# Kernel tuning notes

Measured on AMD Instinct MI355X. Metric: run time of the kernel, lower is better.

Reference implementation:

```python
import jax, jax.numpy as jnp
import numpy as np

D_MODEL = 1024
N_HEADS = 16
D_K = D_MODEL // N_HEADS
D_FF = 4096
LN_EPS = 1e-5


def _layer_norm(x, gamma, beta):
    mu = jnp.mean(x, axis=-1, keepdims=True)
    var = jnp.mean(jnp.square(x - mu), axis=-1, keepdims=True)
    return (x - mu) * jax.lax.rsqrt(var + LN_EPS) * gamma + beta


def setup_inputs() -> dict:
    key = jax.random.key(0)
    ks = jax.random.split(key, 16)
    B, S = 2, 2048
    x = jax.random.normal(ks[0], (B, S, D_MODEL), dtype=jnp.float32)
    # causal mask: True = masked (as used by masked_fill)
    mask = ~jnp.tril(jnp.ones((S, S), dtype=bool))
    s = 1.0 / np.sqrt(D_MODEL)
    sf = 1.0 / np.sqrt(D_FF)
    inp = {
        "x": x,
        "mask": mask,
        "ln1_g": jnp.ones((D_MODEL,), jnp.float32),
        "ln1_b": jnp.zeros((D_MODEL,), jnp.float32),
        "ln2_g": jnp.ones((D_MODEL,), jnp.float32),
        "ln2_b": jnp.zeros((D_MODEL,), jnp.float32),
        "Wq": jax.random.normal(ks[1], (D_MODEL, D_MODEL), jnp.float32) * s,
        "bq": jax.random.normal(ks[2], (D_MODEL,), jnp.float32) * s,
        "Wk": jax.random.normal(ks[3], (D_MODEL, D_MODEL), jnp.float32) * s,
        "bk": jax.random.normal(ks[4], (D_MODEL,), jnp.float32) * s,
        "Wv": jax.random.normal(ks[5], (D_MODEL, D_MODEL), jnp.float32) * s,
        "bv": jax.random.normal(ks[6], (D_MODEL,), jnp.float32) * s,
        "Wo": jax.random.normal(ks[7], (D_MODEL, D_MODEL), jnp.float32) * s,
        "bo": jax.random.normal(ks[8], (D_MODEL,), jnp.float32) * s,
        "W1": jax.random.normal(ks[9], (D_MODEL, D_FF), jnp.float32) * s,
        "b1": jax.random.normal(ks[10], (D_FF,), jnp.float32) * s,
        "W2": jax.random.normal(ks[11], (D_FF, D_MODEL), jnp.float32) * sf,
        "b2": jax.random.normal(ks[12], (D_MODEL,), jnp.float32) * sf,
    }
    return inp


def reference(x, mask, ln1_g, ln1_b, ln2_g, ln2_b,
              Wq, bq, Wk, bk, Wv, bv, Wo, bo, W1, b1, W2, b2):
    B, S, _ = x.shape
    normed = _layer_norm(x, ln1_g, ln1_b)
    # project and split heads: [B, H, S, Dk]
    def split_heads(t):
        return t.reshape(B, S, N_HEADS, D_K).transpose(0, 2, 1, 3)
    Q = split_heads(normed @ Wq + bq)
    K = split_heads(normed @ Wk + bk)
    V = split_heads(normed @ Wv + bv)
    qk = jnp.einsum("bhsd,bhtd->bhst", Q, K)  # [B, H, S, S]
    qk = jnp.where(mask, -jnp.inf, qk)  # mask applied BEFORE scaling, as in source
    attn = jax.nn.softmax(qk / np.sqrt(D_K), axis=-1)
    attn_out = jnp.einsum("bhst,bhtd->bhsd", attn, V)
    attn_out = attn_out.transpose(0, 2, 1, 3).reshape(B, S, D_MODEL)
    attn_out = attn_out @ Wo + bo
    res = attn_out + x  # dropout_p=0 (eval)
    h = _layer_norm(res, ln2_g, ln2_b)
    h = jax.nn.gelu(h @ W1 + b1, approximate=False)
    h = h @ W2 + b2
    return res + h
```

## Files before the change

### kernel.cpp

```cpp
#include <hip/hip_runtime.h>


typedef __bf16 bf16;
typedef __bf16 bf16x8 __attribute__((ext_vector_type(8)));
typedef float f32x4 __attribute__((ext_vector_type(4)));

#define NROWS 4096
#define DM 1024
#define SEQ 2048
#define NHEAD 16
#define DKH 64
#define DFF 4096
#define QSCALE 0.18033688f

#define GLL16(gptr, lptr) \
  __builtin_amdgcn_global_load_lds((const __attribute__((address_space(1))) void*)(gptr), \
                                   (__attribute__((address_space(3))) void*)(lptr), 16, 0, 0)

static char* g_scratch = nullptr;
namespace {
struct ScratchInit {
  ScratchInit() {
    void* p = nullptr;
    if (hipMalloc(&p, (size_t)128 * 1024 * 1024) == hipSuccess) g_scratch = (char*)p;
  }
};
static ScratchInit g_scratch_init;
}

__global__ __launch_bounds__(256) void ln_kernel(const float* __restrict__ inp,
                                                 const float* __restrict__ gamma,
                                                 const float* __restrict__ beta,
                                                 bf16* __restrict__ out) {
  int row = blockIdx.x;
  int t = threadIdx.x;
  float4 xv = *((const float4*)(inp + (size_t)row * DM) + t);
  float v[4] = {xv.x, xv.y, xv.z, xv.w};
  float s = 0.f, sq = 0.f;
#pragma unroll
  for (int i = 0; i < 4; i++) { s += v[i]; sq += v[i] * v[i]; }
#pragma unroll
  for (int m = 32; m >= 1; m >>= 1) { s += __shfl_xor(s, m); sq += __shfl_xor(sq, m); }
  __shared__ float rs[4], rq[4];
  int w = t >> 6, lane = t & 63;
  if (lane == 0) { rs[w] = s; rq[w] = sq; }
  __syncthreads();
  s = rs[0] + rs[1] + rs[2] + rs[3];
  sq = rq[0] + rq[1] + rq[2] + rq[3];
  float mu = s * (1.f / DM);
  float var = sq * (1.f / DM) - mu * mu;
  float rinv = rsqrtf(var + 1e-5f);
  float4 gv = *((const float4*)gamma + t);
  float4 bv = *((const float4*)beta + t);
  float g[4] = {gv.x, gv.y, gv.z, gv.w}, b[4] = {bv.x, bv.y, bv.z, bv.w};
  bf16 ov[4];
#pragma unroll
  for (int i = 0; i < 4; i++) ov[i] = (bf16)((v[i] - mu) * rinv * g[i] + b[i]);
  *(uint2*)(out + (size_t)row * DM + t * 4) = *(uint2*)ov;
}

__global__ __launch_bounds__(256) void concat_bias(const float* __restrict__ bq,
                                                   const float* __restrict__ bk,
                                                   const float* __restrict__ bv,
                                                   float* __restrict__ cat) {
  int i = blockIdx.x * 256 + threadIdx.x;
  float v = (i < 1024) ? bq[i] : (i < 2048 ? bk[i - 1024] : bv[i - 2048]);
  cat[i] = v;
}

__global__ __launch_bounds__(1024) void transpose_f32_bf16(const float* __restrict__ in,
                                                           bf16* __restrict__ out,
                                                           int R, int C) {
  __shared__ bf16 tile[32][33];
  int x = blockIdx.x * 32 + threadIdx.x;
  int y = blockIdx.y * 32 + threadIdx.y;
  tile[threadIdx.y][threadIdx.x] = (bf16)in[(size_t)y * C + x];
  __syncthreads();
  int ox = blockIdx.y * 32 + threadIdx.x;
  int oy = blockIdx.x * 32 + threadIdx.y;
  out[(size_t)oy * R + ox] = tile[threadIdx.x][threadIdx.y];
}

__global__ __launch_bounds__(1024) void transpose_bf16(const bf16* __restrict__ in,
                                                       bf16* __restrict__ out,
                                                       int R, int C) {
  __shared__ bf16 tile[32][33];
  size_t zoff = (size_t)blockIdx.z * (size_t)R * (size_t)C;
  int x = blockIdx.x * 32 + threadIdx.x;
  int y = blockIdx.y * 32 + threadIdx.y;
  tile[threadIdx.y][threadIdx.x] = in[zoff + (size_t)y * C + x];
  __syncthreads();
  int ox = blockIdx.y * 32 + threadIdx.x;
  int oy = blockIdx.x * 32 + threadIdx.y;
  out[zoff + (size_t)oy * R + ox] = tile[threadIdx.x][threadIdx.y];
}

#define BM 128
#define BK 64

#define EPI_QKV3 0
#define EPI_ATTN_RES 1
#define EPI_GELU 2
#define EPI_FFN2 3

template<int EPI, int BNT, int SWZ>
__global__ __launch_bounds__(256, 2) void gemm_bt(
    const bf16* __restrict__ A, const bf16* __restrict__ Bt,
    const float* __restrict__ bias, int Kd, int N,
    bf16* __restrict__ outb, float* __restrict__ outf,
    const float* __restrict__ add) {
  constexpr int MS = (BNT == 128) ? 4 : 2;
  __shared__ bf16 As[BM * BK];
  __shared__ bf16 Bs[BNT * BK];
  int t = threadIdx.x;
  int bx, by;
  if (SWZ) {
    int NXT = gridDim.x, NYT = gridDim.y;
    int L = blockIdx.x + NXT * blockIdx.y;
    int xcd = L & 7, i = L >> 3;
    int RX = NXT >> 1, RY = NYT >> 2;
    bx = (xcd & 1) * RX + (i % RX);
    by = (xcd >> 1) * RY + (i / RX);
  } else {
    bx = blockIdx.x; by = blockIdx.y;
  }
  int m0 = by * BM, n0 = bx * BNT;
  int w = t >> 6, lane = t & 63, ln = lane & 15, quad = lane >> 4;
  int wm = (BNT == 128) ? (w >> 1) * 64 : w * 32;
  int wn = (BNT == 128) ? (w & 1) * 64 : 0;
  f32x4 acc[MS][4];
#pragma unroll
  for (int i2 = 0; i2 < MS; i2++)
#pragma unroll
    for (int j = 0; j < 4; j++) acc[i2][j] = (f32x4){0.f, 0.f, 0.f, 0.f};

  int lr = (t >> 3) & 7, lc = t & 7;
  int gcol = ((lc ^ lr) * 8);
  const bf16* Ab = A + (size_t)(m0 + w * 8 + lr) * Kd + gcol;
  const bf16* Bb = Bt + (size_t)(n0 + w * 8 + lr) * Kd + gcol;
  bf16* AsW = As + (w * 8) * BK;
  bf16* BsW = Bs + (w * 8) * BK;

  for (int k0 = 0; k0 < Kd; k0 += BK) {
    __syncthreads();
#pragma unroll
    for (int j = 0; j < 4; j++)
      GLL16(Ab + (size_t)(32 * j) * Kd + k0, AsW + 32 * j * BK);
#pragma unroll
    for (int j = 0; j < BNT / 32; j++)
      GLL16(Bb + (size_t)(32 * j) * Kd + k0, BsW + 32 * j * BK);
    __syncthreads();
#pragma unroll
    for (int kk = 0; kk < 2; kk++) {
      bf16x8 af[MS], bfr[4];
#pragma unroll
      for (int ms = 0; ms < MS; ms++) {
        int r = wm + ms * 16 + ln;
        af[ms] = *(const bf16x8*)(As + r * BK + (((kk * 4 + quad) ^ (r & 7)) * 8));
      }
#pragma unroll
      for (int ns = 0; ns < 4; ns++) {
        int r = wn + ns * 16 + ln;
        bfr[ns] = *(const bf16x8*)(Bs + r * BK + (((kk * 4 + quad) ^ (r & 7)) * 8));
      }
#pragma unroll
      for (int ms = 0; ms < MS; ms++)
#pragma unroll
        for (int ns = 0; ns < 4; ns++)
          acc[ms][ns] = __builtin_amdgcn_mfma_f32_16x16x32_bf16(af[ms], bfr[ns], acc[ms][ns], 0, 0, 0);
    }
  }

#pragma unroll
  for (int ms = 0; ms < MS; ms++) {
#pragma unroll
    for (int ns = 0; ns < 4; ns++) {
      int col = n0 + wn + ns * 16 + ln;
      float bv = bias[col];
#pragma unroll
      for (int r = 0; r < 4; r++) {
        int row = m0 + wm + ms * 16 + quad * 4 + r;
        float val = acc[ms][ns][r] + bv;
        if (EPI == EPI_QKV3) {
          int which = col >> 10, cc = col & 1023;
          int h = cc >> 6, dk = cc & 63;
          float sc = (which == 0) ? QSCALE : 1.f;
          int b = row >> 11, sx = row & 2047;
          outb[(size_t)which * (4 << 20) +
               ((((size_t)b * NHEAD + h) * SEQ) + sx) * DKH + dk] = (bf16)(val * sc);
        } else if (EPI == EPI_ATTN_RES) {
          size_t idx = (size_t)row * DM + col;
          outf[idx] = val + add[idx];
        } else if (EPI == EPI_GELU) {
          float gl = 0.5f * val * (1.f + erff(val * 0.7071067811865475f));
          outb[(size_t)row * N + col] = (bf16)gl;
        } else {
          size_t idx = (size_t)row * DM + col;
          outf[idx] = val + add[idx];
        }
      }
    }
  }
}

#define LSTR 72
#define OSTR 68

__global__ __launch_bounds__(256) void attn_kernel(
    const bf16* __restrict__ Q, const bf16* __restrict__ K,
    const bf16* __restrict__ Vt, bf16* __restrict__ out) {
  __shared__ float smem[9216];
  int lin = blockIdx.x;
  int bh = lin & 31;
  int jp = 31 - (lin >> 5);
  int t = threadIdx.x, w = t >> 6, lane = t & 63, ln = lane & 15, quad = lane >> 4;
  int qbase = jp * 64;
  size_t bhS = (size_t)bh * SEQ;
  const bf16* Vg0 = Vt + (size_t)bh * DKH * SEQ;
  bf16* Pw = (bf16*)smem + w * 64 * LSTR;

  bf16x8 qa[2][2][2];
#pragma unroll
  for (int u = 0; u < 2; u++)
#pragma unroll
    for (int m = 0; m < 2; m++)
#pragma unroll
      for (int ks = 0; ks < 2; ks++)
        qa[u][m][ks] = *(const bf16x8*)(Q + (bhS + qbase + u * 32 + m * 16 + ln) * DKH + ks * 32 + quad * 8);

  bf16x8 ones;
#pragma unroll
  for (int i = 0; i < 8; i++) ones[i] = (bf16)1.0f;

  f32x4 o[2][2][4];
#pragma unroll
  for (int u = 0; u < 2; u++)
#pragma unroll
    for (int m = 0; m < 2; m++)
#pragma unroll
      for (int i = 0; i < 4; i++) o[u][m][i] = (f32x4){0.f, 0.f, 0.f, 0.f};
  f32x4 accl[2][2];
#pragma unroll
  for (int u = 0; u < 2; u++)
#pragma unroll
    for (int m = 0; m < 2; m++) accl[u][m] = (f32x4){0.f, 0.f, 0.f, 0.f};

  int ktmax = jp;
  for (int kt = w; kt <= ktmax; kt += 4) {
    const bf16* Kg = K + (bhS + kt * 64) * DKH;
    bf16x8 kbf[8], vbf[8];
#pragma unroll
    for (int ns = 0; ns < 4; ns++)
#pragma unroll
      for (int ks = 0; ks < 2; ks++)
        kbf[ns * 2 + ks] = *(const bf16x8*)(Kg + (ns * 16 + ln) * DKH + ks * 32 + quad * 8);
#pragma unroll
    for (int ns = 0; ns < 4; ns++)
#pragma unroll
      for (int ks = 0; ks < 2; ks++)
        vbf[ns * 2 + ks] = *(const bf16x8*)(Vg0 + (size_t)(ns * 16 + ln) * SEQ + kt * 64 + ks * 32 + quad * 8);

#pragma unroll
    for (int u = 0; u < 2; u++) {
      f32x4 s[2][4];
#pragma unroll
      for (int m = 0; m < 2; m++)
#pragma unroll
        for (int ns = 0; ns < 4; ns++) s[m][ns] = (f32x4){0.f, 0.f, 0.f, 0.f};
#pragma unroll
      for (int ns = 0; ns < 4; ns++)
#pragma unroll
        for (int m = 0; m < 2; m++) {
          s[m][ns] = __builtin_amdgcn_mfma_f32_16x16x32_bf16(qa[u][m][0], kbf[ns * 2], s[m][ns], 0, 0, 0);
          s[m][ns] = __builtin_amdgcn_mfma_f32_16x16x32_bf16(qa[u][m][1], kbf[ns * 2 + 1], s[m][ns], 0, 0, 0);
        }
      if (kt == ktmax) {
#pragma unroll
        for (int m = 0; m < 2; m++)
#pragma unroll
          for (int ns = 0; ns < 4; ns++)
#pragma unroll
            for (int r = 0; r < 4; r++) {
              int qrow = qbase + u * 32 + m * 16 + quad * 4 + r;
              int kpos = kt * 64 + ns * 16 + ln;
              if (kpos > qrow) s[m][ns][r] = -30000.f;
            }
      }
#pragma unroll
      for (int m = 0; m < 2; m++)
#pragma unroll
        for (int ns = 0; ns < 4; ns++)
#pragma unroll
          for (int r = 0; r < 4; r++)
            Pw[(u * 32 + m * 16 + quad * 4 + r) * LSTR + ns * 16 + ln] =
                (bf16)__builtin_amdgcn_exp2f(s[m][ns][r]);
    }
    bf16x8 pa[2][2][2];
#pragma unroll
    for (int u = 0; u < 2; u++)
#pragma unroll
      for (int m = 0; m < 2; m++) {
        pa[u][m][0] = *(const bf16x8*)(Pw + (u * 32 + m * 16 + ln) * LSTR + quad * 8);
        pa[u][m][1] = *(const bf16x8*)(Pw + (u * 32 + m * 16 + ln) * LSTR + 32 + quad * 8);
      }
#pragma unroll
    for (int u = 0; u < 2; u++)
#pragma unroll
      for (int m = 0; m < 2; m++) {
        accl[u][m] = __builtin_amdgcn_mfma_f32_16x16x32_bf16(pa[u][m][0], ones, accl[u][m], 0, 0, 0);
        accl[u][m] = __builtin_amdgcn_mfma_f32_16x16x32_bf16(pa[u][m][1], ones, accl[u][m], 0, 0, 0);
      }
#pragma unroll
    for (int ns2 = 0; ns2 < 4; ns2++)
#pragma unroll
      for (int u = 0; u < 2; u++)
#pragma unroll
        for (int m = 0; m < 2; m++) {
          o[u][m][ns2] = __builtin_amdgcn_mfma_f32_16x16x32_bf16(pa[u][m][0], vbf[ns2 * 2], o[u][m][ns2], 0, 0, 0);
          o[u][m][ns2] = __builtin_amdgcn_mfma_f32_16x16x32_bf16(pa[u][m][1], vbf[ns2 * 2 + 1], o[u][m][ns2], 0, 0, 0);
        }
  }

  constexpr int SLAB = 64 * OSTR;
  float* Ob = smem;
  float* Lb = smem + 2 * SLAB;
  __syncthreads();
#pragma unroll
  for (int u = 0; u < 2; u++)
#pragma unroll
    for (int m = 0; m < 2; m++) {
      if (w < 2) {
#pragma unroll
        for (int ns2 = 0; ns2 < 4; ns2++)
#pragma unroll
          for (int r = 0; r < 4; r++)
            Ob[w * SLAB + (u * 32 + m * 16 + quad * 4 + r) * OSTR + ns2 * 16 + ln] = o[u][m][ns2][r];
      }
      if (ln == 0) {
#pragma unroll
        for (int r = 0; r < 4; r++) Lb[w * 64 + u * 32 + m * 16 + quad * 4 + r] = accl[u][m][r];
      }
    }
  __syncthreads();
  if (w >= 2) {
#pragma unroll
    for (int u = 0; u < 2; u++)
#pragma unroll
      for (int m = 0; m < 2; m++)
#pragma unroll
        for (int ns2 = 0; ns2 < 4; ns2++)
#pragma unroll
          for (int r = 0; r < 4; r++) {
            int idx = (w - 2) * SLAB + (u * 32 + m * 16 + quad * 4 + r) * OSTR + ns2 * 16 + ln;
            Ob[idx] += o[u][m][ns2][r];
          }
  }
  __syncthreads();

  int r32 = t >> 3, c0 = (t & 7) * 8;
  int b = bh >> 4, h = bh & 15;
#pragma unroll
  for (int u = 0; u < 2; u++) {
    int row = u * 32 + r32;
    float l = Lb[row] + Lb[64 + row] + Lb[128 + row] + Lb[192 + row];
    float inv = 1.f / l;
    bf16 ov[8];
#pragma unroll
    for (int j = 0; j < 8; j++) {
      float v = Ob[row * OSTR + c0 + j] + Ob[SLAB + row * OSTR + c0 + j];
      ov[j] = (bf16)(v * inv);
    }
    *(uint4*)(out + ((size_t)b * SEQ + qbase + row) * DM + h * DKH + c0) = *(uint4*)ov;
  }
}

extern "C" void kernel_launch(void* const* d_in, const int* in_sizes, int n_in,
                              void* d_out, int out_size, void* d_ws, size_t ws_size,
                              hipStream_t stream) {
  const float* x    = (const float*)d_in[0];
  const float* ln1g = (const float*)d_in[2];
  const float* ln1b = (const float*)d_in[3];
  const float* ln2g = (const float*)d_in[4];
  const float* ln2b = (const float*)d_in[5];
  const float* Wq = (const float*)d_in[6];   const float* bq = (const float*)d_in[7];
  const float* Wk = (const float*)d_in[8];   const float* bk = (const float*)d_in[9];
  const float* Wv = (const float*)d_in[10];  const float* bv = (const float*)d_in[11];
  const float* Wo = (const float*)d_in[12];  const float* bo = (const float*)d_in[13];
  const float* W1 = (const float*)d_in[14];  const float* b1 = (const float*)d_in[15];
  const float* W2 = (const float*)d_in[16];  const float* b2 = (const float*)d_in[17];
  float* outp = (float*)d_out;

  char* scratch = g_scratch ? g_scratch : (char*)d_ws;

  bf16* Wqt = (bf16*)scratch;
  bf16* Wkt = Wqt + (1 << 20);
  bf16* Wvt = Wkt + (1 << 20);
  bf16* Wot = Wvt + (1 << 20);
  bf16* W1t = Wot + (1 << 20);
  bf16* W2t = W1t + (4 << 20);
  bf16* normed = W2t + (4 << 20);
  bf16* Qb = normed + (4 << 20);
  bf16* Kb = Qb + (4 << 20);
  bf16* Vb = Kb + (4 << 20);
  bf16* Vtb = Vb + (4 << 20);
  bf16* attn_o = Vtb + (4 << 20);
  float* resf = (float*)(attn_o + (4 << 20));
  float* bias_cat = resf + (4 << 20);
  bf16* h1 = Qb;

  dim3 b256(256), b1k(32, 32);

  ln_kernel<<<NROWS, b256, 0, stream>>>(x, ln1g, ln1b, normed);
  concat_bias<<<12, b256, 0, stream>>>(bq, bk, bv, bias_cat);

  transpose_f32_bf16<<<dim3(32, 32), b1k, 0, stream>>>(Wq, Wqt, 1024, 1024);
  transpose_f32_bf16<<<dim3(32, 32), b1k, 0, stream>>>(Wk, Wkt, 1024, 1024);
  transpose_f32_bf16<<<dim3(32, 32), b1k, 0, stream>>>(Wv, Wvt, 1024, 1024);
  transpose_f32_bf16<<<dim3(32, 32), b1k, 0, stream>>>(Wo, Wot, 1024, 1024);
  transpose_f32_bf16<<<dim3(128, 32), b1k, 0, stream>>>(W1, W1t, 1024, 4096);
  transpose_f32_bf16<<<dim3(32, 128), b1k, 0, stream>>>(W2, W2t, 4096, 1024);

  gemm_bt<EPI_QKV3, 128, 0><<<dim3(24, 32), b256, 0, stream>>>(
      normed, Wqt, bias_cat, 1024, 3072, Qb, nullptr, nullptr);

  transpose_bf16<<<dim3(2, 64, 32), b1k, 0, stream>>>(Vb, Vtb, 2048, 64);

  attn_kernel<<<dim3(1024), b256, 0, stream>>>(Qb, Kb, Vtb, attn_o);

  gemm_bt<EPI_ATTN_RES, 64, 0><<<dim3(16, 32), b256, 0, stream>>>(
      attn_o, Wot, bo, 1024, 1024, nullptr, resf, x);

  ln_kernel<<<NROWS, b256, 0, stream>>>(resf, ln2g, ln2b, normed);

  gemm_bt<EPI_GELU, 128, 0><<<dim3(32, 32), b256, 0, stream>>>(
      normed, W1t, b1, 1024, 4096, h1, nullptr, nullptr);

  gemm_bt<EPI_FFN2, 64, 1><<<dim3(16, 32), b256, 0, stream>>>(
      h1, W2t, b2, 4096, 1024, nullptr, outp, resf);
}
```

Baseline: 391.9 us.

## Keep attention probabilities in registers via transposed QK^T and permuted V layout

The QK^T MFMA now takes K as the A operand and Q as the B operand, so each lane holds four consecutive key positions for one query row. That matches the B-operand layout needed for the P·V MFMA, so the probabilities are packed straight into bf16x8 registers with v_cvt_pk_bf16_f32. This removes the per-wave LDS round-trip for P and one block barrier. The V transpose kernel now writes its columns in a permuted order so the V fragments line up with the register-packed P ordering. The change relies on exact MFMA lane mappings, so an index mismatch would silently give wrong results.

```diff
diff --git a/kernel.cpp b/kernel.cpp
--- a/kernel.cpp
+++ b/kernel.cpp
@@ -26,6 +26,12 @@
   }
 };
 static ScratchInit g_scratch_init;
+}
+
+__device__ inline unsigned cvt_pk_bf16(float lo, float hi) {
+  unsigned r;
+  asm("v_cvt_pk_bf16_f32 %0, %1, %2" : "=v"(r) : "v"(lo), "v"(hi));
+  return r;
 }
 
 __global__ __launch_bounds__(256) void ln_kernel(const float* __restrict__ inp,
@@ -81,9 +87,9 @@
   out[(size_t)oy * R + ox] = tile[threadIdx.x][threadIdx.y];
 }
 
-__global__ __launch_bounds__(1024) void transpose_bf16(const bf16* __restrict__ in,
-                                                       bf16* __restrict__ out,
-                                                       int R, int C) {
+__global__ __launch_bounds__(1024) void transpose_bf16_vperm(const bf16* __restrict__ in,
+                                                             bf16* __restrict__ out,
+                                                             int R, int C) {
   __shared__ bf16 tile[32][33];
   size_t zoff = (size_t)blockIdx.z * (size_t)R * (size_t)C;
   int x = blockIdx.x * 32 + threadIdx.x;
@@ -92,7 +98,8 @@
   __syncthreads();
   int ox = blockIdx.y * 32 + threadIdx.x;
   int oy = blockIdx.x * 32 + threadIdx.y;
-  out[zoff + (size_t)oy * R + ox] = tile[threadIdx.x][threadIdx.y];
+  int oxp = (ox & ~31) | (((ox >> 2) & 3) << 3) | (((ox >> 4) & 1) << 2) | (ox & 3);
+  out[zoff + (size_t)oy * R + oxp] = tile[threadIdx.x][threadIdx.y];
 }
 
 #define BM 128
@@ -203,13 +210,12 @@
   }
 }
 
-#define LSTR 72
 #define OSTR 68
 
 __global__ __launch_bounds__(256) void attn_kernel(
     const bf16* __restrict__ Q, const bf16* __restrict__ K,
     const bf16* __restrict__ Vt, bf16* __restrict__ out) {
-  __shared__ float smem[9216];
+  __shared__ float smem[2 * 64 * OSTR + 256];
   int lin = blockIdx.x;
   int bh = lin & 31;
   int jp = 31 - (lin >> 5);
@@ -217,7 +223,6 @@
   int qbase = jp * 64;
   size_t bhS = (size_t)bh * SEQ;
   const bf16* Vg0 = Vt + (size_t)bh * DKH * SEQ;
-  bf16* Pw = (bf16*)smem + w * 64 * LSTR;
 
   bf16x8 qa[2][2][2];
 #pragma unroll
@@ -260,6 +265,7 @@
       for (int ks = 0; ks < 2; ks++)
         vbf[ns * 2 + ks] = *(const bf16x8*)(Vg0 + (size_t)(ns * 16 + ln) * SEQ + kt * 64 + ks * 32 + quad * 8);
 
+    bf16x8 pa[2][2][2];
 #pragma unroll
     for (int u = 0; u < 2; u++) {
       f32x4 s[2][4];
@@ -271,8 +277,8 @@
       for (int ns = 0; ns < 4; ns++)
 #pragma unroll
         for (int m = 0; m < 2; m++) {
-          s[m][ns] = __builtin_amdgcn_mfma_f32_16x16x32_bf16(qa[u][m][0], kbf[ns * 2], s[m][ns], 0, 0, 0);
-          s[m][ns] = __builtin_amdgcn_mfma_f32_16x16x32_bf16(qa[u][m][1], kbf[ns * 2 + 1], s[m][ns], 0, 0, 0);
+          s[m][ns] = __builtin_amdgcn_mfma_f32_16x16x32_bf16(kbf[ns * 2], qa[u][m][0], s[m][ns], 0, 0, 0);
+          s[m][ns] = __builtin_amdgcn_mfma_f32_16x16x32_bf16(kbf[ns * 2 + 1], qa[u][m][1], s[m][ns], 0, 0, 0);
         }
       if (kt == ktmax) {
 #pragma unroll
@@ -281,8 +287,8 @@
           for (int ns = 0; ns < 4; ns++)
 #pragma unroll
             for (int r = 0; r < 4; r++) {
-              int qrow = qbase + u * 32 + m * 16 + quad * 4 + r;
-              int kpos = kt * 64 + ns * 16 + ln;
+              int qrow = qbase + u * 32 + m * 16 + ln;
+              int kpos = kt * 64 + ns * 16 + quad * 4 + r;
               if (kpos > qrow) s[m][ns][r] = -30000.f;
             }
       }
@@ -292,17 +298,19 @@
         for (int ns = 0; ns < 4; ns++)
 #pragma unroll
           for (int r = 0; r < 4; r++)
-            Pw[(u * 32 + m * 16 + quad * 4 + r) * LSTR + ns * 16 + ln] =
-                (bf16)__builtin_amdgcn_exp2f(s[m][ns][r]);
+            s[m][ns][r] = __builtin_amdgcn_exp2f(s[m][ns][r]);
+#pragma unroll
+      for (int m = 0; m < 2; m++)
+#pragma unroll
+        for (int j = 0; j < 2; j++) {
+          union { bf16x8 v; unsigned uu[4]; } pk;
+          pk.uu[0] = cvt_pk_bf16(s[m][2 * j][0], s[m][2 * j][1]);
+          pk.uu[1] = cvt_pk_bf16(s[m][2 * j][2], s[m][2 * j][3]);
+          pk.uu[2] = cvt_pk_bf16(s[m][2 * j + 1][0], s[m][2 * j + 1][1]);
+          pk.uu[3] = cvt_pk_bf16(s[m][2 * j + 1][2], s[m][2 * j + 1][3]);
+          pa[u][m][j] = pk.v;
+        }
     }
-    bf16x8 pa[2][2][2];
-#pragma unroll
-    for (int u = 0; u < 2; u++)
-#pragma unroll
-      for (int m = 0; m < 2; m++) {
-        pa[u][m][0] = *(const bf16x8*)(Pw + (u * 32 + m * 16 + ln) * LSTR + quad * 8);
-        pa[u][m][1] = *(const bf16x8*)(Pw + (u * 32 + m * 16 + ln) * LSTR + 32 + quad * 8);
-      }
 #pragma unroll
     for (int u = 0; u < 2; u++)
 #pragma unroll
@@ -324,7 +332,6 @@
   constexpr int SLAB = 64 * OSTR;
   float* Ob = smem;
   float* Lb = smem + 2 * SLAB;
-  __syncthreads();
 #pragma unroll
   for (int u = 0; u < 2; u++)
 #pragma unroll
@@ -423,7 +430,7 @@
   gemm_bt<EPI_QKV3, 128, 0><<<dim3(24, 32), b256, 0, stream>>>(
       normed, Wqt, bias_cat, 1024, 3072, Qb, nullptr, nullptr);
 
-  transpose_bf16<<<dim3(2, 64, 32), b1k, 0, stream>>>(Vb, Vtb, 2048, 64);
+  transpose_bf16_vperm<<<dim3(2, 64, 32), b1k, 0, stream>>>(Vb, Vtb, 2048, 64);
 
   attn_kernel<<<dim3(1024), b256, 0, stream>>>(Qb, Kb, Vtb, attn_o);
 
```

Result: faster. 375.7 us (-4.1%).
